# Performance work log

Measured on AMD Instinct MI355X. Metric: run time of the kernel, lower is better.

## Reference

```python
import jax, jax.numpy as jnp
import numpy as np

N_VARS, N_FACT, N_EDGES, D = 100000, 50000, 1000000, 128


def setup_inputs() -> dict:
    key = jax.random.key(0)
    ks = jax.random.split(key, 8)
    variables = jax.random.normal(ks[0], (N_VARS, D), dtype=jnp.float32)
    factors = jax.random.normal(ks[1], (N_FACT, D), dtype=jnp.float32)
    v_to_f = jax.random.randint(ks[2], (N_EDGES,), 0, N_VARS, dtype=jnp.int32)
    f_to_v = jax.random.randint(ks[3], (N_EDGES,), 0, N_FACT, dtype=jnp.int32)
    edge_attr = jax.random.normal(ks[4], (N_EDGES,), dtype=jnp.float32)
    # small init scale to keep activations sane
    W_msg = jax.random.normal(ks[5], (2 * D + 1, D), dtype=jnp.float32) * 0.05
    b_msg = jnp.zeros((D,), dtype=jnp.float32)
    W_comb = jax.random.normal(ks[6], (2 * D, D), dtype=jnp.float32) * 0.05
    b_comb = jnp.zeros((D,), dtype=jnp.float32)
    return dict(variables=variables, factors=factors, v_to_f=v_to_f,
                f_to_v=f_to_v, edge_attr=edge_attr, W_msg=W_msg, b_msg=b_msg,
                W_comb=W_comb, b_comb=b_comb)


def reference(variables, factors, v_to_f, f_to_v, edge_attr, W_msg, b_msg, W_comb, b_comb):
    # gather endpoint features per edge
    x_i = variables[v_to_f]                      # [E, D]
    x_j = factors[f_to_v]                        # [E, D]
    ea = jnp.zeros_like(edge_attr)[:, None]      # forward passes zeros_like(edge_attr)
    # per-edge message MLP (Linear + activation)
    m = jax.nn.relu(jnp.concatenate([x_i, x_j, ea], axis=-1) @ W_msg + b_msg)  # [E, D]
    # scatter-aggregate messages onto the variable (sender) nodes
    aggr_m = jax.ops.segment_sum(m, v_to_f, num_segments=variables.shape[0])   # [N_v, D]
    # concat + combine MLP + residual
    h = jax.nn.relu(jnp.concatenate([variables, aggr_m], axis=-1) @ W_comb + b_comb)
    return variables + h
```

## Files before the change

### kernel.cpp

```cpp
#include <hip/hip_runtime.h>

#define NV 100000
#define NF 50000
#define NE 1000000
#define MAXDEG 32
#define SCB2 1954
#define GMV 391
#define GMF 196
#define GFN 391

typedef unsigned short ushort_t;
typedef unsigned int uint_t;
typedef __attribute__((ext_vector_type(8))) short bf16x8;
typedef __attribute__((ext_vector_type(8))) _Float16 f16x8;
typedef __attribute__((ext_vector_type(2))) _Float16 f16x2;
typedef __attribute__((ext_vector_type(4))) float f32x4;
typedef __attribute__((ext_vector_type(4))) uint_t u32x4;


__device__ inline ushort_t f2bf(float x) {
    union { float f; uint_t u; } c; c.f = x;
    uint_t r = c.u + 0x7fffu + ((c.u >> 16) & 1u);
    return (ushort_t)(r >> 16);
}

__device__ inline uint_t packh2(float a, float b) {
    auto h = __builtin_amdgcn_cvt_pkrtz(a, b);
    return __builtin_bit_cast(uint_t, h);
}

__device__ inline bf16x8 cvt_frag(float4 lo, float4 hi) {
    uint_t a, b, c, d;
    asm("v_cvt_pk_bf16_f32 %0, %1, %2" : "=v"(a) : "v"(lo.x), "v"(lo.y));
    asm("v_cvt_pk_bf16_f32 %0, %1, %2" : "=v"(b) : "v"(lo.z), "v"(lo.w));
    asm("v_cvt_pk_bf16_f32 %0, %1, %2" : "=v"(c) : "v"(hi.x), "v"(hi.y));
    asm("v_cvt_pk_bf16_f32 %0, %1, %2" : "=v"(d) : "v"(hi.z), "v"(hi.w));
    u32x4 q = {a, b, c, d};
    return __builtin_bit_cast(bf16x8, q);
}

__device__ inline void gload_lds16(const void* g, void* l) {
    __builtin_amdgcn_global_load_lds(
        (const __attribute__((address_space(1))) void*)g,
        (__attribute__((address_space(3))) void*)l, 16, 0, 0);
}

__global__ __launch_bounds__(256) void init_k(const float* __restrict__ Wm,
                                              const float* __restrict__ Wc,
                                              ushort_t* __restrict__ frag,
                                              int* __restrict__ deg) {
    int t = blockIdx.x * 256 + threadIdx.x;
    if (t < NV) deg[t] = 0;
    int t2 = t + 65536;
    if (t2 < NV) deg[t2] = 0;

    int mat = t >> 14;
    int idx = t & 16383;
    int k = idx >> 7, n = idx & 127;
    int srck = k;
    if (mat == 3) {
        int j = k >> 1;
        srck = (j & 15) + 32 * (j >> 4) + 16 * (k & 1);
    }
    const float* src = (mat < 2) ? (Wm + (size_t)mat * 16384) : (Wc + (size_t)(mat - 2) * 16384);
    float v = src[(size_t)srck * 128 + n];
    ushort_t outv;
    if (mat == 3) {
        _Float16 h = (_Float16)v;
        outv = __builtin_bit_cast(ushort_t, h);
    } else {
        outv = f2bf(v);
    }
    int kc = k >> 5, kk = k & 31, quad = kk >> 3, j = kk & 7;
    int ct = n >> 4, np = n & 15, lane = np + 16 * quad;
    frag[(size_t)mat * 16384 + (size_t)((kc * 8 + ct) * 64 + lane) * 8 + j] = outv;
}

__global__ __launch_bounds__(256, 4) void scatter_gemm(const float* __restrict__ V,
                                                       const float* __restrict__ F,
                                                       const ushort_t* __restrict__ wfm,
                                                       const float* __restrict__ bias,
                                                       uint_t* __restrict__ u,
                                                       uint_t* __restrict__ w,
                                                       const int* __restrict__ vtf,
                                                       const int* __restrict__ ftv,
                                                       int* __restrict__ deg,
                                                       ushort_t* __restrict__ sf) {
    if (blockIdx.x >= GMV + GMF) {
        int e2 = (blockIdx.x - (GMV + GMF)) * 256 + threadIdx.x;
        if (e2 < NE / 2) {
            int2 v = *(const int2*)(vtf + (size_t)e2 * 2);
            int2 f = *(const int2*)(ftv + (size_t)e2 * 2);
            int s0 = atomicAdd(&deg[v.x], 1);
            if (s0 < MAXDEG) sf[(size_t)v.x * MAXDEG + s0] = (ushort_t)f.x;
            int s1 = atomicAdd(&deg[v.y], 1);
            if (s1 < MAXDEG) sf[(size_t)v.y * MAXDEG + s1] = (ushort_t)f.y;
        }
        return;
    }
    __shared__ ushort_t Bs[16384];

    const float* A; const ushort_t* wf; uint_t* C; const float* bs; int M, r0;
    if (blockIdx.x < GMV) { A = V; wf = wfm;         C = u; bs = bias;    M = NV; r0 = blockIdx.x * 256; }
    else                  { A = F; wf = wfm + 16384; C = w; bs = nullptr; M = NF; r0 = (blockIdx.x - GMV) * 256; }

    const int wv = threadIdx.x >> 6;
    const int lane = threadIdx.x & 63;
    const int quad = lane >> 4, np = lane & 15;

    {
        const char* gsrc = (const char*)wf;
        char* lbase = (char*)Bs;
        int toff = threadIdx.x * 16;
#pragma unroll
        for (int i = 0; i < 8; i++) gload_lds16(gsrc + i * 4096 + toff, lbase + i * 4096 + toff);
    }

    float4 vlo[4], vhi[4];
    {
        int ar0 = r0 + wv * 16 + np; if (ar0 >= M) ar0 = M - 1;
        const float* ap = A + (size_t)ar0 * 128 + quad * 8;
#pragma unroll
        for (int kc = 0; kc < 4; kc++) {
            vlo[kc] = *(const float4*)(ap + kc * 32);
            vhi[kc] = *(const float4*)(ap + kc * 32 + 4);
        }
    }
    float bb0[4], bb1[4];
#pragma unroll
    for (int g = 0; g < 4; g++) {
        bb0[g] = bs ? bs[np + 32 * g] : 0.f;
        bb1[g] = bs ? bs[np + 32 * g + 16] : 0.f;
    }

    asm volatile("s_waitcnt vmcnt(0)" ::: "memory");
    __builtin_amdgcn_sched_barrier(0);
    __syncthreads();

#pragma unroll
    for (int t = 0; t < 4; t++) {
        bf16x8 a[4];
#pragma unroll
        for (int kc = 0; kc < 4; kc++) a[kc] = cvt_frag(vlo[kc], vhi[kc]);

        if (t < 3) {
            int nr = r0 + (t + 1) * 64 + wv * 16 + np; if (nr >= M) nr = M - 1;
            const float* ap = A + (size_t)nr * 128 + quad * 8;
#pragma unroll
            for (int kc = 0; kc < 4; kc++) {
                vlo[kc] = *(const float4*)(ap + kc * 32);
                vhi[kc] = *(const float4*)(ap + kc * 32 + 4);
            }
        }
        __builtin_amdgcn_sched_barrier(0);

        f32x4 acc[8];
#pragma unroll
        for (int ct = 0; ct < 8; ct++) acc[ct] = (f32x4){0.f, 0.f, 0.f, 0.f};
#pragma unroll
        for (int kc = 0; kc < 4; kc++) {
            const ushort_t* wp = Bs + (size_t)(kc * 8 * 64 + lane) * 8;
#pragma unroll
            for (int ct = 0; ct < 8; ct++) {
                bf16x8 b = *(const bf16x8*)(wp + ct * 512);
                acc[ct] = __builtin_amdgcn_mfma_f32_16x16x32_bf16(a[kc], b, acc[ct], 0, 0, 0);
            }
        }

#pragma unroll
        for (int g = 0; g < 4; g++) {
#pragma unroll
            for (int r = 0; r < 4; r++) {
                int orow = r0 + t * 64 + wv * 16 + quad * 4 + r;
                if (orow < M)
                    C[(size_t)orow * 64 + g * 16 + np] = packh2(acc[2 * g][r] + bb0[g],
                                                                acc[2 * g + 1][r] + bb1[g]);
            }
        }
    }
}

__global__ __launch_bounds__(256, 6) void aggregate(const uint_t* __restrict__ u32,
                                                    const uint_t* __restrict__ w32,
                                                    const int* __restrict__ deg,
                                                    const ushort_t* __restrict__ sf,
                                                    uint_t* __restrict__ aggr32) {
    int v = (blockIdx.x * 256 + threadIdx.x) >> 6;
    int lane = threadIdx.x & 63;
    if (v >= NV) return;
    int cnt = deg[v]; if (cnt > MAXDEG) cnt = MAXDEG;
    int i0 = v * MAXDEG, i1 = i0 + cnt;
    f16x2 uh = __builtin_bit_cast(f16x2, u32[(size_t)v * 64 + lane]);
    const f16x2 z2 = __builtin_bit_cast(f16x2, 0u);
    f16x2 acc[8];
#pragma unroll
    for (int j = 0; j < 8; j++) acc[j] = z2;
    for (int i = i0; i < i1; i += 8) {
        int f[8];
#pragma unroll
        for (int j = 0; j < 8; j++) {
            int idx = i + j; if (idx > i1 - 1) idx = i1 - 1;
            f[j] = sf[idx];
        }
        uint_t p[8];
#pragma unroll
        for (int j = 0; j < 8; j++) p[j] = w32[(size_t)f[j] * 64 + lane];
#pragma unroll
        for (int j = 0; j < 8; j++) {
            uint_t pj = (i + j < i1) ? p[j] : 0xFC00FC00u;
            f16x2 s = uh + __builtin_bit_cast(f16x2, pj);
            f16x2 r;
            asm("v_pk_max_f16 %0, %1, %2" : "=v"(r) : "v"(s), "v"(z2));
            acc[j] += r;
        }
    }
    f16x2 t0 = (acc[0] + acc[1]) + (acc[2] + acc[3]);
    f16x2 t1 = (acc[4] + acc[5]) + (acc[6] + acc[7]);
    f16x2 tt = t0 + t1;
    aggr32[(size_t)v * 64 + lane] = __builtin_bit_cast(uint_t, tt);
}

__global__ __launch_bounds__(512, 4) void gemm_final(const float* __restrict__ V,
                                                     const ushort_t* __restrict__ aggr,
                                                     const ushort_t* __restrict__ wfc,
                                                     const float* __restrict__ bias,
                                                     float* __restrict__ OUT, int M) {
    __shared__ ushort_t Bs[32768];

    const int wv = threadIdx.x >> 6;
    const int lane = threadIdx.x & 63;
    const int quad = lane >> 4, np = lane & 15;
    const int r0 = blockIdx.x * 256;

    {
        const char* gsrc = (const char*)wfc;
        char* lbase = (char*)Bs;
        int toff = threadIdx.x * 16;
#pragma unroll
        for (int i = 0; i < 8; i++) gload_lds16(gsrc + i * 8192 + toff, lbase + i * 8192 + toff);
    }

    float4 vlo[4], vhi[4];
    f16x8 af[4];
    {
        int ar0 = r0 + wv * 16 + np; if (ar0 >= M) ar0 = M - 1;
        const float* ap = V + (size_t)ar0 * 128 + quad * 8;
#pragma unroll
        for (int kc = 0; kc < 4; kc++) {
            vlo[kc] = *(const float4*)(ap + kc * 32);
            vhi[kc] = *(const float4*)(ap + kc * 32 + 4);
        }
        const ushort_t* agp = aggr + (size_t)ar0 * 128 + quad * 8;
#pragma unroll
        for (int kc = 0; kc < 4; kc++) af[kc] = *(const f16x8*)(agp + kc * 32);
    }
    float bb[8];
#pragma unroll
    for (int ct = 0; ct < 8; ct++) bb[ct] = bias[ct * 16 + np];

    asm volatile("s_waitcnt vmcnt(0)" ::: "memory");
    __builtin_amdgcn_sched_barrier(0);
    __syncthreads();

#pragma unroll
    for (int t = 0; t < 2; t++) {
        bf16x8 abf[4];
#pragma unroll
        for (int kc = 0; kc < 4; kc++) abf[kc] = cvt_frag(vlo[kc], vhi[kc]);

        if (t < 1) {
            int nr = r0 + 128 + wv * 16 + np; if (nr >= M) nr = M - 1;
            const float* ap = V + (size_t)nr * 128 + quad * 8;
#pragma unroll
            for (int kc = 0; kc < 4; kc++) {
                vlo[kc] = *(const float4*)(ap + kc * 32);
                vhi[kc] = *(const float4*)(ap + kc * 32 + 4);
            }
        }
        __builtin_amdgcn_sched_barrier(0);

        f32x4 acc[8];
#pragma unroll
        for (int ct = 0; ct < 8; ct++) acc[ct] = (f32x4){0.f, 0.f, 0.f, 0.f};

#pragma unroll
        for (int kc = 0; kc < 4; kc++) {
            const ushort_t* wp = Bs + (size_t)(kc * 8 * 64 + lane) * 8;
#pragma unroll
            for (int ct = 0; ct < 8; ct++) {
                bf16x8 b = *(const bf16x8*)(wp + ct * 512);
                acc[ct] = __builtin_amdgcn_mfma_f32_16x16x32_bf16(abf[kc], b, acc[ct], 0, 0, 0);
            }
        }
#pragma unroll
        for (int kc = 0; kc < 4; kc++) {
            const ushort_t* wp = Bs + 16384 + (size_t)(kc * 8 * 64 + lane) * 8;
#pragma unroll
            for (int ct = 0; ct < 8; ct++) {
                f16x8 b = *(const f16x8*)(wp + ct * 512);
                acc[ct] = __builtin_amdgcn_mfma_f32_16x16x32_f16(af[kc], b, acc[ct], 0, 0, 0);
            }
        }
        if (t < 1) {
            int nr = r0 + 128 + wv * 16 + np; if (nr >= M) nr = M - 1;
            const ushort_t* agp = aggr + (size_t)nr * 128 + quad * 8;
#pragma unroll
            for (int kc = 0; kc < 4; kc++) af[kc] = *(const f16x8*)(agp + kc * 32);
        }
        __builtin_amdgcn_sched_barrier(0);

        const int orow0 = r0 + t * 128 + wv * 16 + quad * 4;
        float resid[32];
#pragma unroll
        for (int ct = 0; ct < 8; ct++)
#pragma unroll
            for (int r = 0; r < 4; r++) {
                int orow = orow0 + r;
                resid[ct * 4 + r] = (orow < M) ? V[(size_t)orow * 128 + ct * 16 + np] : 0.f;
            }
#pragma unroll
        for (int ct = 0; ct < 8; ct++)
#pragma unroll
            for (int r = 0; r < 4; r++) {
                int orow = orow0 + r;
                if (orow < M)
                    OUT[(size_t)orow * 128 + ct * 16 + np] =
                        resid[ct * 4 + r] + fmaxf(acc[ct][r] + bb[ct], 0.f);
            }
    }
}

extern "C" void kernel_launch(void* const* d_in, const int* in_sizes, int n_in,
                              void* d_out, int out_size, void* d_ws, size_t ws_size,
                              hipStream_t stream) {
    const float* variables = (const float*)d_in[0];
    const float* factors   = (const float*)d_in[1];
    const int*   v_to_f    = (const int*)d_in[2];
    const int*   f_to_v    = (const int*)d_in[3];
    const float* W_msg     = (const float*)d_in[5];
    const float* b_msg     = (const float*)d_in[6];
    const float* W_comb    = (const float*)d_in[7];
    const float* b_comb    = (const float*)d_in[8];
    float* out = (float*)d_out;

    ushort_t* wfrag = (ushort_t*)d_ws;
    uint_t*   u     = (uint_t*)(wfrag + 4 * 16384);
    uint_t*   w     = u + (size_t)NV * 64;
    uint_t*   aggr  = w + (size_t)NF * 64;
    int*      deg   = (int*)(aggr + (size_t)NV * 64);
    ushort_t* sf    = (ushort_t*)d_out;

    init_k<<<256, 256, 0, stream>>>(W_msg, W_comb, wfrag, deg);

    scatter_gemm<<<GMV + GMF + SCB2, 256, 0, stream>>>(variables, factors, wfrag, b_msg,
                                                       u, w, v_to_f, f_to_v, deg, sf);

    aggregate<<<(NV * 64) / 256, 256, 0, stream>>>(u, w, deg, sf, aggr);

    gemm_final<<<GFN, 512, 0, stream>>>(variables, (const ushort_t*)aggr, wfrag + 2 * 16384,
                                        b_comb, out, NV);
}
```

Before: 258.3 us.

## Fuse neighbor aggregation into final combine GEMM via shared-memory staging

Merges the separate aggregate kernel into the final GEMM kernel. Each 512-thread block first computes aggregated messages for its 128 rows into padded LDS, then runs the MFMA combine, so the aggr buffer is never written to or read back from global memory and one launch disappears. The edge list sf moves from the output buffer into workspace, because the output is now written in the same kernel that reads sf. In exchange each block handles fewer rows, uses more LDS (which may lower occupancy), and its GEMM cannot start until all eight waves finish the irregular gather phase.

```diff
diff --git a/kernel.cpp b/kernel.cpp
--- a/kernel.cpp
+++ b/kernel.cpp
@@ -7,7 +7,8 @@
 #define SCB2 1954
 #define GMV 391
 #define GMF 196
-#define GFN 391
+#define GFN2 782
+#define AGSTRIDE 68
 
 typedef unsigned short ushort_t;
 typedef unsigned int uint_t;
@@ -180,57 +181,21 @@
     }
 }
 
-__global__ __launch_bounds__(256, 6) void aggregate(const uint_t* __restrict__ u32,
-                                                    const uint_t* __restrict__ w32,
-                                                    const int* __restrict__ deg,
-                                                    const ushort_t* __restrict__ sf,
-                                                    uint_t* __restrict__ aggr32) {
-    int v = (blockIdx.x * 256 + threadIdx.x) >> 6;
-    int lane = threadIdx.x & 63;
-    if (v >= NV) return;
-    int cnt = deg[v]; if (cnt > MAXDEG) cnt = MAXDEG;
-    int i0 = v * MAXDEG, i1 = i0 + cnt;
-    f16x2 uh = __builtin_bit_cast(f16x2, u32[(size_t)v * 64 + lane]);
-    const f16x2 z2 = __builtin_bit_cast(f16x2, 0u);
-    f16x2 acc[8];
-#pragma unroll
-    for (int j = 0; j < 8; j++) acc[j] = z2;
-    for (int i = i0; i < i1; i += 8) {
-        int f[8];
-#pragma unroll
-        for (int j = 0; j < 8; j++) {
-            int idx = i + j; if (idx > i1 - 1) idx = i1 - 1;
-            f[j] = sf[idx];
-        }
-        uint_t p[8];
-#pragma unroll
-        for (int j = 0; j < 8; j++) p[j] = w32[(size_t)f[j] * 64 + lane];
-#pragma unroll
-        for (int j = 0; j < 8; j++) {
-            uint_t pj = (i + j < i1) ? p[j] : 0xFC00FC00u;
-            f16x2 s = uh + __builtin_bit_cast(f16x2, pj);
-            f16x2 r;
-            asm("v_pk_max_f16 %0, %1, %2" : "=v"(r) : "v"(s), "v"(z2));
-            acc[j] += r;
-        }
-    }
-    f16x2 t0 = (acc[0] + acc[1]) + (acc[2] + acc[3]);
-    f16x2 t1 = (acc[4] + acc[5]) + (acc[6] + acc[7]);
-    f16x2 tt = t0 + t1;
-    aggr32[(size_t)v * 64 + lane] = __builtin_bit_cast(uint_t, tt);
-}
-
-__global__ __launch_bounds__(512, 4) void gemm_final(const float* __restrict__ V,
-                                                     const ushort_t* __restrict__ aggr,
-                                                     const ushort_t* __restrict__ wfc,
-                                                     const float* __restrict__ bias,
-                                                     float* __restrict__ OUT, int M) {
-    __shared__ ushort_t Bs[32768];
+__global__ __launch_bounds__(512) void agg_final(const float* __restrict__ V,
+                                                 const uint_t* __restrict__ u32,
+                                                 const uint_t* __restrict__ w32,
+                                                 const int* __restrict__ deg,
+                                                 const ushort_t* __restrict__ sf,
+                                                 const ushort_t* __restrict__ wfc,
+                                                 const float* __restrict__ bias,
+                                                 float* __restrict__ OUT, int M) {
+    __shared__ ushort_t Bs[32768 + 128 * AGSTRIDE * 2];
 
     const int wv = threadIdx.x >> 6;
     const int lane = threadIdx.x & 63;
     const int quad = lane >> 4, np = lane & 15;
-    const int r0 = blockIdx.x * 256;
+    const int r0 = blockIdx.x * 128;
+    uint_t* Agg = (uint_t*)(Bs + 32768);
 
     {
         const char* gsrc = (const char*)wfc;
@@ -239,9 +204,7 @@
 #pragma unroll
         for (int i = 0; i < 8; i++) gload_lds16(gsrc + i * 8192 + toff, lbase + i * 8192 + toff);
     }
-
     float4 vlo[4], vhi[4];
-    f16x8 af[4];
     {
         int ar0 = r0 + wv * 16 + np; if (ar0 >= M) ar0 = M - 1;
         const float* ap = V + (size_t)ar0 * 128 + quad * 8;
@@ -250,84 +213,102 @@
             vlo[kc] = *(const float4*)(ap + kc * 32);
             vhi[kc] = *(const float4*)(ap + kc * 32 + 4);
         }
-        const ushort_t* agp = aggr + (size_t)ar0 * 128 + quad * 8;
+    }
+    float bb[8];
+#pragma unroll
+    for (int ct = 0; ct < 8; ct++) bb[ct] = bias[ct * 16 + np];
+
+    const f16x2 z2 = __builtin_bit_cast(f16x2, 0u);
+
+    for (int it = 0; it < 16; ++it) {
+        int row = it * 8 + wv;
+        int vc = r0 + row; if (vc >= M) vc = M - 1;
+        int cnt = deg[vc]; if (cnt > MAXDEG) cnt = MAXDEG;
+        f16x2 uh = __builtin_bit_cast(f16x2, u32[(size_t)vc * 64 + lane]);
+        const ushort_t* sfp = sf + (size_t)vc * MAXDEG;
+        f16x2 acc8[8];
+#pragma unroll
+        for (int j = 0; j < 8; j++) acc8[j] = z2;
+        for (int i = 0; i < cnt; i += 8) {
+            int f[8];
+#pragma unroll
+            for (int j = 0; j < 8; j++) {
+                int idx = i + j; if (idx > cnt - 1) idx = cnt - 1;
+                f[j] = sfp[idx];
+            }
+            uint_t p[8];
+#pragma unroll
+            for (int j = 0; j < 8; j++) p[j] = w32[(size_t)f[j] * 64 + lane];
+#pragma unroll
+            for (int j = 0; j < 8; j++) {
+                uint_t pj = (i + j < cnt) ? p[j] : 0xFC00FC00u;
+                f16x2 s = uh + __builtin_bit_cast(f16x2, pj);
+                f16x2 r;
+                asm("v_pk_max_f16 %0, %1, %2" : "=v"(r) : "v"(s), "v"(z2));
+                acc8[j] += r;
+            }
+        }
+        f16x2 t0 = (acc8[0] + acc8[1]) + (acc8[2] + acc8[3]);
+        f16x2 t1 = (acc8[4] + acc8[5]) + (acc8[6] + acc8[7]);
+        f16x2 tt = t0 + t1;
+        Agg[row * AGSTRIDE + lane] = __builtin_bit_cast(uint_t, tt);
+    }
+
+    asm volatile("s_waitcnt vmcnt(0)" ::: "memory");
+    __syncthreads();
+
+    bf16x8 abf[4];
+#pragma unroll
+    for (int kc = 0; kc < 4; kc++) abf[kc] = cvt_frag(vlo[kc], vhi[kc]);
+
+    f16x8 af[4];
+    {
+        const ushort_t* agp = (const ushort_t*)Agg + (size_t)(wv * 16 + np) * (AGSTRIDE * 2) + quad * 8;
 #pragma unroll
         for (int kc = 0; kc < 4; kc++) af[kc] = *(const f16x8*)(agp + kc * 32);
     }
-    float bb[8];
-#pragma unroll
-    for (int ct = 0; ct < 8; ct++) bb[ct] = bias[ct * 16 + np];
-
-    asm volatile("s_waitcnt vmcnt(0)" ::: "memory");
-    __builtin_amdgcn_sched_barrier(0);
-    __syncthreads();
-
-#pragma unroll
-    for (int t = 0; t < 2; t++) {
-        bf16x8 abf[4];
-#pragma unroll
-        for (int kc = 0; kc < 4; kc++) abf[kc] = cvt_frag(vlo[kc], vhi[kc]);
-
-        if (t < 1) {
-            int nr = r0 + 128 + wv * 16 + np; if (nr >= M) nr = M - 1;
-            const float* ap = V + (size_t)nr * 128 + quad * 8;
-#pragma unroll
-            for (int kc = 0; kc < 4; kc++) {
-                vlo[kc] = *(const float4*)(ap + kc * 32);
-                vhi[kc] = *(const float4*)(ap + kc * 32 + 4);
-            }
-        }
-        __builtin_amdgcn_sched_barrier(0);
-
-        f32x4 acc[8];
-#pragma unroll
-        for (int ct = 0; ct < 8; ct++) acc[ct] = (f32x4){0.f, 0.f, 0.f, 0.f};
-
-#pragma unroll
-        for (int kc = 0; kc < 4; kc++) {
-            const ushort_t* wp = Bs + (size_t)(kc * 8 * 64 + lane) * 8;
-#pragma unroll
-            for (int ct = 0; ct < 8; ct++) {
-                bf16x8 b = *(const bf16x8*)(wp + ct * 512);
-                acc[ct] = __builtin_amdgcn_mfma_f32_16x16x32_bf16(abf[kc], b, acc[ct], 0, 0, 0);
-            }
-        }
-#pragma unroll
-        for (int kc = 0; kc < 4; kc++) {
-            const ushort_t* wp = Bs + 16384 + (size_t)(kc * 8 * 64 + lane) * 8;
-#pragma unroll
-            for (int ct = 0; ct < 8; ct++) {
-                f16x8 b = *(const f16x8*)(wp + ct * 512);
-                acc[ct] = __builtin_amdgcn_mfma_f32_16x16x32_f16(af[kc], b, acc[ct], 0, 0, 0);
-            }
-        }
-        if (t < 1) {
-            int nr = r0 + 128 + wv * 16 + np; if (nr >= M) nr = M - 1;
-            const ushort_t* agp = aggr + (size_t)nr * 128 + quad * 8;
-#pragma unroll
-            for (int kc = 0; kc < 4; kc++) af[kc] = *(const f16x8*)(agp + kc * 32);
-        }
-        __builtin_amdgcn_sched_barrier(0);
-
-        const int orow0 = r0 + t * 128 + wv * 16 + quad * 4;
-        float resid[32];
-#pragma unroll
-        for (int ct = 0; ct < 8; ct++)
-#pragma unroll
-            for (int r = 0; r < 4; r++) {
-                int orow = orow0 + r;
-                resid[ct * 4 + r] = (orow < M) ? V[(size_t)orow * 128 + ct * 16 + np] : 0.f;
-            }
-#pragma unroll
-        for (int ct = 0; ct < 8; ct++)
-#pragma unroll
-            for (int r = 0; r < 4; r++) {
-                int orow = orow0 + r;
-                if (orow < M)
-                    OUT[(size_t)orow * 128 + ct * 16 + np] =
-                        resid[ct * 4 + r] + fmaxf(acc[ct][r] + bb[ct], 0.f);
-            }
-    }
+
+    f32x4 acc[8];
+#pragma unroll
+    for (int ct = 0; ct < 8; ct++) acc[ct] = (f32x4){0.f, 0.f, 0.f, 0.f};
+
+#pragma unroll
+    for (int kc = 0; kc < 4; kc++) {
+        const ushort_t* wp = Bs + (size_t)(kc * 8 * 64 + lane) * 8;
+#pragma unroll
+        for (int ct = 0; ct < 8; ct++) {
+            bf16x8 b = *(const bf16x8*)(wp + ct * 512);
+            acc[ct] = __builtin_amdgcn_mfma_f32_16x16x32_bf16(abf[kc], b, acc[ct], 0, 0, 0);
+        }
+    }
+#pragma unroll
+    for (int kc = 0; kc < 4; kc++) {
+        const ushort_t* wp = Bs + 16384 + (size_t)(kc * 8 * 64 + lane) * 8;
+#pragma unroll
+        for (int ct = 0; ct < 8; ct++) {
+            f16x8 b = *(const f16x8*)(wp + ct * 512);
+            acc[ct] = __builtin_amdgcn_mfma_f32_16x16x32_f16(af[kc], b, acc[ct], 0, 0, 0);
+        }
+    }
+
+    const int orow0 = r0 + wv * 16 + quad * 4;
+    float resid[32];
+#pragma unroll
+    for (int ct = 0; ct < 8; ct++)
+#pragma unroll
+        for (int r = 0; r < 4; r++) {
+            int orow = orow0 + r;
+            resid[ct * 4 + r] = (orow < M) ? V[(size_t)orow * 128 + ct * 16 + np] : 0.f;
+        }
+#pragma unroll
+    for (int ct = 0; ct < 8; ct++)
+#pragma unroll
+        for (int r = 0; r < 4; r++) {
+            int orow = orow0 + r;
+            if (orow < M)
+                OUT[(size_t)orow * 128 + ct * 16 + np] =
+                    resid[ct * 4 + r] + fmaxf(acc[ct][r] + bb[ct], 0.f);
+        }
 }
 
 extern "C" void kernel_launch(void* const* d_in, const int* in_sizes, int n_in,
@@ -346,17 +327,14 @@
     ushort_t* wfrag = (ushort_t*)d_ws;
     uint_t*   u     = (uint_t*)(wfrag + 4 * 16384);
     uint_t*   w     = u + (size_t)NV * 64;
-    uint_t*   aggr  = w + (size_t)NF * 64;
-    int*      deg   = (int*)(aggr + (size_t)NV * 64);
-    ushort_t* sf    = (ushort_t*)d_out;
+    int*      deg   = (int*)(w + (size_t)NF * 64);
+    ushort_t* sf    = (ushort_t*)(deg + NV);
 
     init_k<<<256, 256, 0, stream>>>(W_msg, W_comb, wfrag, deg);
 
     scatter_gemm<<<GMV + GMF + SCB2, 256, 0, stream>>>(variables, factors, wfrag, b_msg,
                                                        u, w, v_to_f, f_to_v, deg, sf);
 
-    aggregate<<<(NV * 64) / 256, 256, 0, stream>>>(u, w, deg, sf, aggr);
-
-    gemm_final<<<GFN, 512, 0, stream>>>(variables, (const ushort_t*)aggr, wfrag + 2 * 16384,
+    agg_final<<<GFN2, 512, 0, stream>>>(variables, u, w, deg, sf, wfrag + 2 * 16384,
                                         b_comb, out, NV);
 }
```

New measurement: 324.3 us. 25.5% more time.
